# Optimization experiments

Hardware: AMD Instinct MI355X
Metric: run time of the kernel (lower is better)

The kernel has to match this reference:

```python
import jax, jax.numpy as jnp
import numpy as np


def setup_inputs() -> dict:
    key = jax.random.key(0)
    ks = jax.random.split(key, 6)
    N, D, E = 512, 16, 12
    X = jax.random.normal(ks[0], (N, D), jnp.float32)
    Y = jax.random.normal(ks[1], (N, E), jnp.float32)
    m = jax.random.normal(ks[2], (1, D), jnp.float32)
    A = jax.random.normal(ks[3], (D, D), jnp.float32)
    s = A @ A.T / D + 0.5 * jnp.eye(D, dtype=jnp.float32)  # SPD state covariance
    lengthscale = 0.5 + 1.5 * jax.random.uniform(ks[4], (E, D), jnp.float32)  # ARD lengthscales [E,D]
    outputscale = jnp.full((E,), 0.001, jnp.float32)  # Interval(0.001, 0.001001) constraint
    noise = 0.05 + 0.1 * jax.random.uniform(ks[5], (E,), jnp.float32)
    return {"X": X, "Y": Y, "m": m, "s": s,
            "lengthscale": lengthscale, "outputscale": outputscale, "noise": noise}


def _moment_match(X, Y, m, s, lengthscale, outputscale, noise):
    N, D = X.shape
    E = Y.shape[1]
    eyeD = jnp.eye(D, dtype=X.dtype)
    eyeN = jnp.eye(N, dtype=X.dtype)

    # --- standardization (torch std is unbiased, ddof=1) ---
    X_mean = jnp.mean(X, axis=0, keepdims=True)           # [1,D]
    X_std = jnp.std(X, axis=0, ddof=1, keepdims=True)     # [1,D]
    Yt = Y.T                                              # [E,N]
    Y_mean = jnp.mean(Yt, axis=-1, keepdims=True)         # [E,1]
    Y_std = jnp.std(Yt, axis=-1, ddof=1, keepdims=True)   # [E,1]
    Xs = (X - X_mean) / X_std                             # [N,D]
    Yn = (Yt - Y_mean) / Y_std                            # [E,N]

    inv_s = jnp.linalg.inv(s)
    mm = (m - X_mean) / X_std                             # [1,D]
    ss = s / (X_std.T * X_std)                            # [D,D]

    # --- calculate_factorizations ---
    diff = Xs[:, None, :] - Xs[None, :, :]                # [N,N,D]
    sq = jnp.sum((diff[None, :, :, :] / lengthscale[:, None, None, :]) ** 2, -1)  # [E,N,N]
    K = outputscale[:, None, None] * jnp.exp(-0.5 * sq)   # [E,N,N]
    A = K + noise[:, None, None] * eyeN                   # [E,N,N]
    iK = jnp.linalg.solve(A, jnp.broadcast_to(eyeN, (E, N, N)))  # [E,N,N]
    beta = jnp.linalg.solve(A, Yn[:, :, None])[:, :, 0]   # [E,N]

    # --- predict_given_factorizations ---
    inp = Xs - mm                                         # [N,D] centralized inputs
    iN = inp[None, :, :] / lengthscale[:, None, :]        # [E,N,D]
    ls2 = lengthscale ** 2                                # [E,D]
    # B = iL @ s @ iL + I
    B = ss[None, :, :] / (lengthscale[:, :, None] * lengthscale[:, None, :]) + eyeD  # [E,D,D]
    t = jnp.swapaxes(jnp.linalg.solve(B, jnp.swapaxes(iN, 1, 2)), 1, 2)  # [E,N,D]
    lb = jnp.exp(-0.5 * jnp.sum(iN * t, -1)) * beta       # [E,N]
    tiL = t / lengthscale[:, None, :]                     # [E,N,D]
    c = outputscale / jnp.sqrt(jnp.linalg.det(B))         # [E]
    M = (jnp.sum(lb, -1) * c)[:, None]                    # [E,1]
    V = jnp.einsum('end,en->ed', tiL, lb) * c[:, None]    # [E,D]

    # cross terms over output pairs (a,b)
    R0diag = 1.0 / ls2[None, :, :] + 1.0 / ls2[:, None, :]          # [E,E,D]
    R = ss[None, None, :, :] * R0diag[:, :, None, :] + eyeD          # s @ diag(r) + I, [E,E,D,D]
    X1 = inp[None, None, :, :] / ls2[:, None, None, :]               # [E,1,N,D]
    X2 = -inp[None, None, :, :] / ls2[None, :, None, :]              # [1,E,N,D]
    Q = jnp.linalg.solve(R, jnp.broadcast_to(ss, (E, E, D, D))) / 2  # [E,E,D,D]
    X1Q = X1 @ Q                                                     # [E,E,N,D]
    X2Q = X2 @ Q                                                     # [E,E,N,D]
    Xs_ = jnp.sum(X1Q * X1, -1)                                      # [E,E,N]
    X2s = jnp.sum(X2Q * X2, -1)                                      # [E,E,N]
    maha = -2.0 * (X1Q @ jnp.swapaxes(jnp.broadcast_to(X2, (E, E, N, D)), -1, -2)) \
        + Xs_[:, :, :, None] + X2s[:, :, None, :]                    # [E,E,N,N]
    kvec = jnp.log(outputscale)[:, None] - 0.5 * jnp.sum(iN ** 2, -1)  # [E,N]
    L = jnp.exp(kvec[:, None, :, None] + kvec[None, :, None, :] + maha)  # [E,E,N,N]
    S = jnp.einsum('an,abnm,bm->ab', beta, L, beta)                  # [E,E]
    diagL = L[jnp.arange(E), jnp.arange(E)]                          # [E,N,N]
    S = S - jnp.diag(jnp.sum(iK * diagL, axis=(1, 2)))
    S = S / jnp.sqrt(jnp.linalg.det(R))
    S = S + jnp.diag(outputscale)
    S = S - M @ M.T

    Mout = M.T                                                       # [1,E]
    Vout = V.T                                                       # [D,E]

    # --- de-standardize ---
    Mout = Mout * Y_std.T + Y_mean.T
    S = S * (Y_std * Y_std.T)
    var = jnp.concatenate([X_std, Y_std.T], axis=-1)                 # [1,D+E]
    mask_var = var.T * var                                           # [D+E,D+E]
    cov = (ss @ Vout) * mask_var[:D, D:]                             # [D,E]
    Vout = inv_s @ cov
    return Mout, S, Vout


def reference(X, Y, m, s, lengthscale, outputscale, noise):
    return _moment_match(X, Y, m, s, lengthscale, outputscale, noise)
```

## Files before the change

kernel.cpp:

```cpp
#include <hip/hip_runtime.h>
#include <math.h>

constexpr int N = 512;
constexpr int D = 16;
constexpr int E = 12;
constexpr int NPAIR = E*(E+1)/2;

constexpr size_t OFF_A     = 0;
constexpr size_t OFF_IK    = OFF_A    + (size_t)E*N*N;
constexpr size_t OFF_XS    = OFF_IK   + (size_t)E*N*N;
constexpr size_t OFF_INP   = OFF_XS   + (size_t)N*D;
constexpr size_t OFF_YN    = OFF_INP  + (size_t)N*D;
constexpr size_t OFF_BETA  = OFF_YN   + (size_t)E*N;
constexpr size_t OFF_KVEC  = OFF_BETA + (size_t)E*N;
constexpr size_t OFF_LB    = OFF_KVEC + (size_t)E*N;
constexpr size_t OFF_TIL   = OFF_LB   + (size_t)E*N;
constexpr size_t OFF_U     = OFF_TIL  + (size_t)E*N*D;
constexpr size_t OFF_V     = OFF_U    + (size_t)E*E*N;
constexpr size_t OFF_Q     = OFF_V    + (size_t)E*E*N;
constexpr size_t OFF_BINV  = OFF_Q    + (size_t)E*E*D*D;
constexpr size_t OFF_C     = OFF_BINV + (size_t)E*D*D;
constexpr size_t OFF_ISDR  = OFF_C    + E;
constexpr size_t OFF_SPART = OFF_ISDR + E*E;
constexpr size_t OFF_TPART = OFF_SPART+ (size_t)E*E*8;
constexpr size_t OFF_XMEAN = OFF_TPART+ (size_t)E*8;
constexpr size_t OFF_XSTD  = OFF_XMEAN+ D;
constexpr size_t OFF_YMEAN = OFF_XSTD + D;
constexpr size_t OFF_YSTD  = OFF_YMEAN+ E;
constexpr size_t OFF_SSM   = OFF_YSTD + E;
constexpr size_t OFF_P     = OFF_SSM  + D*D;
constexpr size_t OFF_T     = OFF_P    + (size_t)E*1792*64;

__device__ __forceinline__ int prow(int k) { return k*(480 - 32*k); }

__device__ __forceinline__ void pc2ab(int pc, int& a, int& b) {
    int aa = 0, t = pc;
    while (t >= E - aa) { t -= E - aa; ++aa; }
    a = aa; b = aa + t;
}

__device__ __forceinline__ void fact64(float a[16], float (*cb)[64], float* invd, int lane, int wv) {
    #pragma unroll
    for (int k = 0; k < 64; ++k) {
        const int kg = k >> 4, kj = k & 15;
        if (wv == kg) {
            float dkk = __shfl(a[kj], k);
            float dv = sqrtf(dkk);
            float iv = 1.0f / dv;
            float sc = a[kj] * iv;
            if (lane == k)      { a[kj] = dv; invd[k] = iv; }
            else if (lane > k)  a[kj] = sc;
            cb[k & 1][lane] = (lane > k) ? a[kj] : 0.0f;
        }
        __syncthreads();
        float lrk = cb[k & 1][lane];
        #pragma unroll
        for (int j = 0; j < 16; ++j)
            a[j] = fmaf(-lrk, cb[k & 1][wv*16 + j], a[j]);
    }
}

__device__ __forceinline__ void binv64(const float (*Lsh)[65], float (*Xsh)[65],
                                       const float* invd, float (*Tsh)[16][17], int tid) {
    if (tid < 64) {
        int g = tid >> 4, c = tid & 15;
        int b = g*16;
        for (int r = 0; r < c; ++r) Xsh[b+r][b+c] = 0.f;
        for (int r = c; r < 16; ++r) {
            float acc = (r == c) ? 1.0f : 0.0f;
            for (int k = c; k < r; ++k)
                acc = fmaf(-Lsh[b+r][b+k], Xsh[b+k][b+c], acc);
            Xsh[b+r][b+c] = acc * invd[b+r];
        }
    } else {
        const int bis[6] = {0,0,0,1,1,2};
        const int bjs[6] = {1,2,3,2,3,3};
        for (int idx = tid - 64; idx < 1536; idx += 192) {
            int blk = idx >> 8, off = idx & 255;
            Xsh[bis[blk]*16 + (off >> 4)][bjs[blk]*16 + (off & 15)] = 0.f;
        }
    }
    __syncthreads();
    for (int d = 1; d <= 3; ++d) {
        int np = 4 - d;
        for (int idx = tid; idx < np*256; idx += 256) {
            int p = idx >> 8, off = idx & 255;
            int r = off >> 4, c = off & 15;
            int i = p + d, j = p;
            float acc = 0.f;
            for (int k = j; k < i; ++k)
                #pragma unroll
                for (int m = 0; m < 16; ++m)
                    acc = fmaf(Lsh[i*16+r][k*16+m], Xsh[k*16+m][j*16+c], acc);
            Tsh[p][r][c] = acc;
        }
        __syncthreads();
        for (int idx = tid; idx < np*256; idx += 256) {
            int p = idx >> 8, off = idx & 255;
            int r = off >> 4, c = off & 15;
            int i = p + d, j = p;
            float acc = 0.f;
            #pragma unroll
            for (int m = 0; m < 16; ++m)
                acc = fmaf(Xsh[i*16+r][i*16+m], Tsh[p][m][c], acc);
            Xsh[i*16+r][j*16+c] = -acc;
        }
        __syncthreads();
    }
}

__device__ __forceinline__ void load_tile4(const float* __restrict__ g, size_t ldg,
                                           float (*S)[65], int tid) {
    #pragma unroll
    for (int j = 0; j < 4; ++j) {
        int idx = tid + j*256;
        int r = idx >> 4, c4 = idx & 15;
        float4 v = *(const float4*)&g[(size_t)r*ldg + c4*4];
        S[r][c4*4+0] = v.x; S[r][c4*4+1] = v.y; S[r][c4*4+2] = v.z; S[r][c4*4+3] = v.w;
    }
}

__device__ __forceinline__ void xs_body(float* __restrict__ ws, const float* __restrict__ ls,
                                        const float* __restrict__ os, int t, int tid) {
    int pc = t / N, n = t % N;
    int a, b;
    pc2ab(pc, a, b);
    int pairQ = a*E + b;
    __shared__ float Qs[16][17];
    __shared__ float i2a[16], i2b[16];
    Qs[tid >> 4][tid & 15] = ws[OFF_Q + (size_t)pairQ*D*D + tid];
    if (tid < 16) { float l = ls[a*D + tid]; i2a[tid] = 1.0f/(l*l); }
    else if (tid < 32) { int d = tid-16; float l = ls[b*D + d]; i2b[d] = 1.0f/(l*l); }
    __syncthreads();
    float x1[D], x2[D];
    float siNa = 0.f, siNb = 0.f;
    #pragma unroll
    for (int d = 0; d < D; ++d) {
        float ip = ws[OFF_INP + n*D + d];
        x1[d] = ip * i2a[d];
        x2[d] = ip * i2b[d];
        siNa = fmaf(ip*ip, i2a[d], siNa);
        siNb = fmaf(ip*ip, i2b[d], siNb);
    }
    float xs1 = 0.f, xs2 = 0.f;
    #pragma unroll
    for (int j = 0; j < D; ++j) {
        float t1 = 0.f, t2 = 0.f;
        #pragma unroll
        for (int i = 0; i < D; ++i) { t1 = fmaf(x1[i], Qs[i][j], t1); t2 = fmaf(x2[i], Qs[i][j], t2); }
        xs1 = fmaf(t1, x1[j], xs1);
        xs2 = fmaf(t2, x2[j], xs2);
    }
    float loa = logf(os[a]), lob = logf(os[b]);
    ws[OFF_U + (size_t)pc*N + n] = loa - 0.5f*siNa + xs1;
    ws[OFF_V + (size_t)pc*N + n] = lob - 0.5f*siNb + xs2;
}

__device__ __forceinline__ void point_body(float* __restrict__ ws, const float* __restrict__ ls,
                                           int t) {
    int e = t >> 9, n = t & 511;
    float iN[D], tt[D], l[D];
    #pragma unroll
    for (int d = 0; d < D; ++d) { l[d] = ls[e*D + d]; iN[d] = ws[OFF_INP + n*D + d] / l[d]; }
    #pragma unroll
    for (int d = 0; d < D; ++d) {
        float acc = 0.f;
        #pragma unroll
        for (int j = 0; j < D; ++j) acc += ws[OFF_BINV + ((size_t)e*D + d)*D + j] * iN[j];
        tt[d] = acc;
    }
    float siNt = 0.f;
    #pragma unroll
    for (int d = 0; d < D; ++d) siNt += iN[d]*tt[d];
    float lbv = __expf(-0.5f * siNt) * ws[OFF_BETA + e*N + n];
    ws[OFF_LB + e*N + n] = lbv;
    #pragma unroll
    for (int d = 0; d < D; ++d) ws[OFF_TIL + ((size_t)e*N + n)*D + d] = tt[d] / l[d];
}

__global__ __launch_bounds__(512) void k_prep(const float* __restrict__ X, const float* __restrict__ Y,
                                              const float* __restrict__ m, const float* __restrict__ s,
                                              float* __restrict__ ws) {
    int tid = threadIdx.x;
    int lane = tid & 63, wave = tid >> 6;
    __shared__ float meanX[D], stdX[D], meanY[E], stdY[E], mmsh[D];

    for (int col = wave; col < D + E; col += 8) {
        float s1 = 0.f, s2 = 0.f;
        if (col < D) {
            #pragma unroll
            for (int i = 0; i < 8; ++i) { float v = X[(i*64 + lane)*D + col]; s1 += v; s2 += v*v; }
        } else {
            int e = col - D;
            #pragma unroll
            for (int i = 0; i < 8; ++i) { float v = Y[(i*64 + lane)*E + e]; s1 += v; s2 += v*v; }
        }
        #pragma unroll
        for (int off = 32; off > 0; off >>= 1) { s1 += __shfl_xor(s1, off); s2 += __shfl_xor(s2, off); }
        if (lane == 0) {
            float mean = s1 * (1.0f/N);
            float var  = (s2 - (float)N*mean*mean) * (1.0f/(N-1));
            float sd   = sqrtf(var);
            if (col < D) { meanX[col] = mean; stdX[col] = sd; }
            else         { meanY[col-D] = mean; stdY[col-D] = sd; }
        }
    }
    __syncthreads();
    if (tid < D) {
        mmsh[tid] = (m[tid] - meanX[tid]) / stdX[tid];
        ws[OFF_XMEAN + tid] = meanX[tid];
        ws[OFF_XSTD  + tid] = stdX[tid];
    }
    if (tid < E) { ws[OFF_YMEAN + tid] = meanY[tid]; ws[OFF_YSTD + tid] = stdY[tid]; }
    __syncthreads();
    int n = tid;
    #pragma unroll
    for (int d = 0; d < D; ++d) {
        float xs = (X[n*D + d] - meanX[d]) / stdX[d];
        ws[OFF_XS  + n*D + d] = xs;
        ws[OFF_INP + n*D + d] = xs - mmsh[d];
    }
    #pragma unroll
    for (int e = 0; e < E; ++e)
        ws[OFF_YN + e*N + n] = (Y[n*E + e] - meanY[e]) / stdY[e];
    if (tid < D*D) {
        int i = tid / D, j = tid % D;
        ws[OFF_SSM + tid] = s[tid] / (stdX[i] * stdX[j]);
    }
}

__global__ __launch_bounds__(256) void k_buildA(float* __restrict__ ws, const float* __restrict__ ls,
                                                const float* __restrict__ os, const float* __restrict__ noise) {
    int bid = blockIdx.x;
    int tid = threadIdx.x;
    if (bid < E*64) {
        int e  = bid >> 6;
        int t  = bid & 63;
        int bn = t >> 3, bm = t & 7;
        __shared__ float xn[64][17], xm[64][17];
        __shared__ float il2[16];
        for (int idx = tid; idx < 1024; idx += 256) {
            int r = idx >> 4, d0 = idx & 15;
            xn[r][d0] = ws[OFF_XS + (size_t)(bn*64 + r)*D + d0];
            xm[r][d0] = ws[OFF_XS + (size_t)(bm*64 + r)*D + d0];
        }
        if (tid < 16) { float l = ls[e*D + tid]; il2[tid] = 1.0f/(l*l); }
        __syncthreads();
        int tx = tid & 15, ty = tid >> 4;
        float osv = os[e], nsv = noise[e];
        float acc[4][4] = {};
        #pragma unroll
        for (int d = 0; d < 16; ++d) {
            float il = il2[d];
            float an[4], am[4];
            #pragma unroll
            for (int q = 0; q < 4; ++q) { an[q] = xn[ty + q*16][d]; am[q] = xm[tx + q*16][d]; }
            #pragma unroll
            for (int q = 0; q < 4; ++q)
                #pragma unroll
                for (int w = 0; w < 4; ++w) { float df = an[q] - am[w]; acc[q][w] = fmaf(df*df, il, acc[q][w]); }
        }
        float* A = ws + OFF_A + (size_t)e*N*N;
        #pragma unroll
        for (int q = 0; q < 4; ++q)
            #pragma unroll
            for (int w = 0; w < 4; ++w) {
                int nr = bn*64 + ty + q*16, mc = bm*64 + tx + w*16;
                float v = osv * __expf(-0.5f * acc[q][w]);
                if (nr == mc) v += nsv;
                A[(size_t)nr*N + mc] = v;
            }
        return;
    }
    int bidx = bid - E*64;
    int i = tid >> 4, j = tid & 15;
    if (bidx < E) {
        int e = bidx;
        __shared__ float Bm[16][17], BInv[16][17];
        float li = ls[e*D + i], lj = ls[e*D + j];
        Bm[i][j] = ws[OFF_SSM + i*D + j] / (li*lj) + ((i==j) ? 1.f : 0.f);
        BInv[i][j] = (i==j) ? 1.f : 0.f;
        __syncthreads();
        float det = 1.f;
        for (int k = 0; k < D; ++k) {
            float p   = Bm[k][k];
            float fik = Bm[i][k];
            float bkj = Bm[k][j];
            float ikj = BInv[k][j];
            __syncthreads();
            det *= p;
            if (i == k) { Bm[k][j] = bkj/p; BInv[k][j] = ikj/p; }
            else        { float f = fik/p; Bm[i][j] -= f*bkj; BInv[i][j] -= f*ikj; }
            __syncthreads();
        }
        ws[OFF_BINV + ((size_t)e*D + i)*D + j] = BInv[i][j];
        if (tid == 0) ws[OFF_C + e] = os[e] / sqrtf(det);
    } else {
        int pair = bidx - E;
        int a = pair / E, b = pair % E;
        __shared__ float Rm[16][17], RInv[16][17], ssl[16][17];
        float la = ls[a*D + j], lb2 = ls[b*D + j];
        float rj = 1.f/(la*la) + 1.f/(lb2*lb2);
        float ssv = ws[OFF_SSM + i*D + j];
        ssl[i][j] = ssv;
        Rm[i][j] = ssv * rj + ((i==j) ? 1.f : 0.f);
        RInv[i][j] = (i==j) ? 1.f : 0.f;
        __syncthreads();
        float det = 1.f;
        for (int k = 0; k < D; ++k) {
            float p   = Rm[k][k];
            float fik = Rm[i][k];
            float rkj = Rm[k][j];
            float ikj = RInv[k][j];
            __syncthreads();
            det *= p;
            if (i == k) { Rm[k][j] = rkj/p; RInv[k][j] = ikj/p; }
            else        { float f = fik/p; Rm[i][j] -= f*rkj; RInv[i][j] -= f*ikj; }
            __syncthreads();
        }
        float q = 0.f;
        #pragma unroll
        for (int k2 = 0; k2 < D; ++k2) q += RInv[i][k2] * ssl[k2][j];
        ws[OFF_Q + ((size_t)pair*D + i)*D + j] = 0.5f * q;
        if (tid == 0) ws[OFF_ISDR + pair] = 1.f / sqrtf(det);
    }
}

__global__ __launch_bounds__(256) void k_diag64(float* __restrict__ ws, int k0) {
    int e = blockIdx.x;
    int tid = threadIdx.x;
    int lane = tid & 63, wv = tid >> 6;
    const float* A = ws + OFF_A + (size_t)e*N*N;
    float* W = ws + OFF_IK + (size_t)e*N*N;
    __shared__ float Lsh[64][65], Xsh[64][65];
    __shared__ float cb[2][64];
    __shared__ float invd[64];
    __shared__ float Tsh[3][16][17];
    float a[16];
    #pragma unroll
    for (int j = 0; j < 16; ++j)
        a[j] = A[(size_t)(k0 + wv*16 + j)*N + k0 + lane];
    __syncthreads();
    fact64(a, cb, invd, lane, wv);
    #pragma unroll
    for (int j = 0; j < 16; ++j) Lsh[lane][wv*16 + j] = a[j];
    __syncthreads();
    binv64(Lsh, Xsh, invd, Tsh, tid);
    for (int idx = tid; idx < 4096; idx += 256) {
        int r = idx >> 6, c = idx & 63;
        W[(size_t)(k0 + r)*N + k0 + c] = Xsh[r][c];
    }
}

__global__ __launch_bounds__(256) void k_panelmul(float* __restrict__ ws, int k0) {
    int kk = k0 >> 6;
    int nb = (N - k0 - 64) >> 6;
    int e  = blockIdx.x / nb;
    int bi = blockIdx.x % nb;
    float* A = ws + OFF_A + (size_t)e*N*N;
    const float* W = ws + OFF_IK + (size_t)e*N*N;
    int r0 = k0 + 64 + bi*64;
    __shared__ float Ps[64][65], Wsh[64][65];
    int tid = threadIdx.x;
    load_tile4(A + (size_t)r0*N + k0, N, Ps, tid);
    load_tile4(W + (size_t)k0*N + k0, N, Wsh, tid);
    __syncthreads();
    int tx = tid & 15, ty = tid >> 4;
    float acc[4][4] = {};
    #pragma unroll 8
    for (int j = 0; j < 64; ++j) {
        float pr[4], wr[4];
        #pragma unroll
        for (int q = 0; q < 4; ++q) { pr[q] = Ps[ty*4+q][j]; wr[q] = Wsh[tx*4+q][j]; }
        #pragma unroll
        for (int q = 0; q < 4; ++q)
            #pragma unroll
            for (int w = 0; w < 4; ++w) acc[q][w] = fmaf(pr[q], wr[w], acc[q][w]);
    }
    float* Pp = ws + OFF_P + ((size_t)e*1792 + prow(kk) + (size_t)bi*64)*64;
    #pragma unroll
    for (int q = 0; q < 4; ++q)
        #pragma unroll
        for (int w = 0; w < 4; ++w) {
            A[(size_t)(r0 + ty*4 + q)*N + k0 + tx*4 + w] = acc[q][w];
            Pp[(size_t)(ty*4 + q)*64 + tx*4 + w] = acc[q][w];
        }
}

__global__ __launch_bounds__(256) void k_traild(float* __restrict__ ws, int k0) {
    int t0 = k0 + 64;
    int nb = (N - t0) >> 6;
    int ntiles = (nb*(nb+1)) >> 1;
    int e = blockIdx.x / ntiles;
    int t = blockIdx.x % ntiles;
    int bj = 0; while (t >= nb - bj) { t -= nb - bj; ++bj; }
    int bi = bj + t;
    bool same = (bi == bj);
    bool isdiag0 = (bi == 0) && (bj == 0);
    float* A = ws + OFF_A + (size_t)e*N*N;
    __shared__ float Sr[64][65], Sc[64][65];
    __shared__ float cb[2][64];
    __shared__ float invd[64];
    __shared__ float Tsh[3][16][17];
    int tid = threadIdx.x;
    int tx = tid & 15, ty = tid >> 4;
    load_tile4(A + (size_t)(t0 + bi*64)*N + k0, N, Sr, tid);
    if (!same) load_tile4(A + (size_t)(t0 + bj*64)*N + k0, N, Sc, tid);
    __syncthreads();
    float acc[4][4] = {};
    if (same) {
        #pragma unroll 8
        for (int p = 0; p < 64; ++p) {
            float ar[4], ac[4];
            #pragma unroll
            for (int q = 0; q < 4; ++q) { ar[q] = Sr[ty*4+q][p]; ac[q] = Sr[tx*4+q][p]; }
            #pragma unroll
            for (int q = 0; q < 4; ++q)
                #pragma unroll
                for (int w = 0; w < 4; ++w) acc[q][w] = fmaf(ar[q], ac[w], acc[q][w]);
        }
    } else {
        #pragma unroll 8
        for (int p = 0; p < 64; ++p) {
            float ar[4], ac[4];
            #pragma unroll
            for (int q = 0; q < 4; ++q) { ar[q] = Sr[ty*4+q][p]; ac[q] = Sc[tx*4+q][p]; }
            #pragma unroll
            for (int q = 0; q < 4; ++q)
                #pragma unroll
                for (int w = 0; w < 4; ++w) acc[q][w] = fmaf(ar[q], ac[w], acc[q][w]);
        }
    }
    float* Out = A + (size_t)(t0 + bi*64)*N + (t0 + bj*64);
    if (!isdiag0) {
        #pragma unroll
        for (int q = 0; q < 4; ++q)
            #pragma unroll
            for (int w = 0; w < 4; ++w)
                Out[(size_t)(ty*4+q)*N + tx*4+w] -= acc[q][w];
        return;
    }
    __syncthreads();
    #pragma unroll
    for (int q = 0; q < 4; ++q)
        #pragma unroll
        for (int w = 0; w < 4; ++w)
            Sc[ty*4+q][tx*4+w] = Out[(size_t)(ty*4+q)*N + tx*4+w] - acc[q][w];
    __syncthreads();
    int lane = tid & 63, wv = tid >> 6;
    float a[16];
    #pragma unroll
    for (int j = 0; j < 16; ++j) a[j] = Sc[lane][wv*16 + j];
    __syncthreads();
    fact64(a, cb, invd, lane, wv);
    #pragma unroll
    for (int j = 0; j < 16; ++j) Sc[lane][wv*16 + j] = a[j];
    __syncthreads();
    binv64(Sc, Sr, invd, Tsh, tid);
    float* W = ws + OFF_IK + (size_t)e*N*N;
    for (int idx = tid; idx < 4096; idx += 256) {
        int r = idx >> 6, c = idx & 63;
        W[(size_t)(t0 + r)*N + t0 + c] = Sr[r][c];
    }
}

__global__ __launch_bounds__(256) void k_dc1(float* __restrict__ ws) {
    int e = blockIdx.x >> 2, p = blockIdx.x & 3;
    float* W = ws + OFF_IK + (size_t)e*N*N;
    const float* Lt = ws + OFF_P + ((size_t)e*1792 + prow(2*p))*64;
    __shared__ float Sa[64][65], Sb[64][65], T[64][65];
    int tid = threadIdx.x;
    int tx = tid & 15, ty = tid >> 4;
    load_tile4(Lt, 64, Sa, tid);
    load_tile4(W + (size_t)(2*p*64)*N + 2*p*64, N, Sb, tid);
    __syncthreads();
    float acc[4][4] = {};
    #pragma unroll 8
    for (int pp = 0; pp < 64; ++pp) {
        float ar[4], bc[4];
        #pragma unroll
        for (int q = 0; q < 4; ++q) { ar[q] = Sa[ty*4+q][pp]; bc[q] = Sb[pp][tx*4+q]; }
        #pragma unroll
        for (int q = 0; q < 4; ++q)
            #pragma unroll
            for (int w = 0; w < 4; ++w) acc[q][w] = fmaf(ar[q], bc[w], acc[q][w]);
    }
    #pragma unroll
    for (int q = 0; q < 4; ++q)
        #pragma unroll
        for (int w = 0; w < 4; ++w) T[ty*4+q][tx*4+w] = acc[q][w];
    __syncthreads();
    load_tile4(W + (size_t)((2*p+1)*64)*N + (2*p+1)*64, N, Sa, tid);
    __syncthreads();
    float o[4][4] = {};
    #pragma unroll 8
    for (int pp = 0; pp < 64; ++pp) {
        float ar[4], bc[4];
        #pragma unroll
        for (int q = 0; q < 4; ++q) { ar[q] = Sa[ty*4+q][pp]; bc[q] = T[pp][tx*4+q]; }
        #pragma unroll
        for (int q = 0; q < 4; ++q)
            #pragma unroll
            for (int w = 0; w < 4; ++w) o[q][w] = fmaf(ar[q], bc[w], o[q][w]);
    }
    #pragma unroll
    for (int q = 0; q < 4; ++q)
        #pragma unroll
        for (int w = 0; w < 4; ++w)
            W[(size_t)((2*p+1)*64 + ty*4 + q)*N + 2*p*64 + tx*4 + w] = -o[q][w];
}

__global__ __launch_bounds__(256) void k_dcT(float* __restrict__ ws, int H) {
    int per_e = 4*H;
    int e = blockIdx.x / per_e;
    int rem = blockIdx.x % per_e;
    int p  = rem / (H*H);
    int tt = rem % (H*H);
    int ti = tt / H, tj = tt % H;
    int C0 = 2*p*H;
    int I  = C0 + H + ti;
    const float* W = ws + OFF_IK + (size_t)e*N*N;
    float* Tt = ws + OFF_T + (size_t)e*65536 + (size_t)(p*H*H + ti*H + tj)*4096;
    __shared__ float Sa[64][65], Sb[64][65];
    int tid = threadIdx.x;
    int tx = tid & 15, ty = tid >> 4;
    float acc[4][4] = {};
    for (int k = tj; k < H; ++k) {
        int K = C0 + k;
        const float* Lt = ws + OFF_P + ((size_t)e*1792 + prow(K) + (size_t)(I - K - 1)*64)*64;
        __syncthreads();
        load_tile4(Lt, 64, Sa, tid);
        load_tile4(W + (size_t)(K*64)*N + (C0 + tj)*64, N, Sb, tid);
        __syncthreads();
        #pragma unroll 8
        for (int pp = 0; pp < 64; ++pp) {
            float ar[4], bc[4];
            #pragma unroll
            for (int q = 0; q < 4; ++q) { ar[q] = Sa[ty*4+q][pp]; bc[q] = Sb[pp][tx*4+q]; }
            #pragma unroll
            for (int q = 0; q < 4; ++q)
                #pragma unroll
                for (int w = 0; w < 4; ++w) acc[q][w] = fmaf(ar[q], bc[w], acc[q][w]);
        }
    }
    #pragma unroll
    for (int q = 0; q < 4; ++q)
        #pragma unroll
        for (int w = 0; w < 4; ++w)
            Tt[(size_t)(ty*4+q)*64 + tx*4 + w] = acc[q][w];
}

__global__ __launch_bounds__(256) void k_dcW(float* __restrict__ ws, int H) {
    int per_e = 4*H;
    int e = blockIdx.x / per_e;
    int rem = blockIdx.x % per_e;
    int p  = rem / (H*H);
    int tt = rem % (H*H);
    int ti = tt / H, tj = tt % H;
    int C0 = 2*p*H, R0 = C0 + H;
    float* W = ws + OFF_IK + (size_t)e*N*N;
    const float* Tbase = ws + OFF_T + (size_t)e*65536 + (size_t)(p*H*H)*4096;
    __shared__ float Sa[64][65], Sb[64][65];
    int tid = threadIdx.x;
    int tx = tid & 15, ty = tid >> 4;
    float acc[4][4] = {};
    for (int tk = 0; tk <= ti; ++tk) {
        const float* Tt = Tbase + (size_t)(tk*H + tj)*4096;
        __syncthreads();
        load_tile4(W + (size_t)((R0 + ti)*64)*N + (R0 + tk)*64, N, Sa, tid);
        load_tile4(Tt, 64, Sb, tid);
        __syncthreads();
        #pragma unroll 8
        for (int pp = 0; pp < 64; ++pp) {
            float ar[4], bc[4];
            #pragma unroll
            for (int q = 0; q < 4; ++q) { ar[q] = Sa[ty*4+q][pp]; bc[q] = Sb[pp][tx*4+q]; }
            #pragma unroll
            for (int q = 0; q < 4; ++q)
                #pragma unroll
                for (int w = 0; w < 4; ++w) acc[q][w] = fmaf(ar[q], bc[w], acc[q][w]);
        }
    }
    #pragma unroll
    for (int q = 0; q < 4; ++q)
        #pragma unroll
        for (int w = 0; w < 4; ++w)
            W[(size_t)((R0 + ti)*64 + ty*4 + q)*N + (C0 + tj)*64 + tx*4 + w] = -acc[q][w];
}

__global__ __launch_bounds__(256) void k_syrk(float* __restrict__ ws, const float* __restrict__ ls,
                                              const float* __restrict__ os) {
    int tid = threadIdx.x;
    if (blockIdx.x >= E*36) {
        int t = (blockIdx.x - E*36)*256 + tid;
        xs_body(ws, ls, os, t, tid);
        return;
    }
    int e = blockIdx.x / 36;
    int t = blockIdx.x % 36;
    int bj = 0; while (t >= 8 - bj) { t -= 8 - bj; ++bj; }
    int bi = bj + t;
    bool same = (bi == bj);
    const float* W = ws + OFF_IK + (size_t)e*N*N;
    float*      IK = ws + OFF_A  + (size_t)e*N*N;
    __shared__ float Sa[64][65], Sb[64][65];
    int tx = tid & 15, ty = tid >> 4;

    float4 pa[4], pb[4];
    #pragma unroll
    for (int j = 0; j < 4; ++j) {
        int idx = tid + j*256;
        int r = idx >> 4, c4 = idx & 15;
        pa[j] = *(const float4*)&W[(size_t)(bi*64 + r)*N + bi*64 + c4*4];
        if (!same) pb[j] = *(const float4*)&W[(size_t)(bi*64 + r)*N + bj*64 + c4*4];
    }

    float acc[4][4] = {};
    for (int p = bi; p < 8; ++p) {
        __syncthreads();
        #pragma unroll
        for (int j = 0; j < 4; ++j) {
            int idx = tid + j*256;
            int r = idx >> 4, c4 = idx & 15;
            Sa[r][c4*4+0] = pa[j].x; Sa[r][c4*4+1] = pa[j].y; Sa[r][c4*4+2] = pa[j].z; Sa[r][c4*4+3] = pa[j].w;
            if (!same) { Sb[r][c4*4+0] = pb[j].x; Sb[r][c4*4+1] = pb[j].y; Sb[r][c4*4+2] = pb[j].z; Sb[r][c4*4+3] = pb[j].w; }
        }
        if (p < 7) {
            #pragma unroll
            for (int j = 0; j < 4; ++j) {
                int idx = tid + j*256;
                int r = idx >> 4, c4 = idx & 15;
                pa[j] = *(const float4*)&W[(size_t)((p+1)*64 + r)*N + bi*64 + c4*4];
                if (!same) pb[j] = *(const float4*)&W[(size_t)((p+1)*64 + r)*N + bj*64 + c4*4];
            }
        }
        __syncthreads();
        if (same) {
            #pragma unroll 8
            for (int pr2 = 0; pr2 < 64; ++pr2) {
                float ar[4], ac[4];
                #pragma unroll
                for (int q = 0; q < 4; ++q) { ar[q] = Sa[pr2][ty*4+q]; ac[q] = Sa[pr2][tx*4+q]; }
                #pragma unroll
                for (int q = 0; q < 4; ++q)
                    #pragma unroll
                    for (int w = 0; w < 4; ++w) acc[q][w] = fmaf(ar[q], ac[w], acc[q][w]);
            }
        } else {
            #pragma unroll 8
            for (int pr2 = 0; pr2 < 64; ++pr2) {
                float ar[4], ac[4];
                #pragma unroll
                for (int q = 0; q < 4; ++q) { ar[q] = Sa[pr2][ty*4+q]; ac[q] = Sb[pr2][tx*4+q]; }
                #pragma unroll
                for (int q = 0; q < 4; ++q)
                    #pragma unroll
                    for (int w = 0; w < 4; ++w) acc[q][w] = fmaf(ar[q], ac[w], acc[q][w]);
            }
        }
    }
    #pragma unroll
    for (int q = 0; q < 4; ++q)
        #pragma unroll
        for (int w = 0; w < 4; ++w) {
            int r = bi*64 + ty*4 + q, c = bj*64 + tx*4 + w;
            IK[(size_t)r*N + c] = acc[q][w];
            IK[(size_t)c*N + r] = acc[q][w];
        }
}

__global__ __launch_bounds__(256) void k_beta(float* __restrict__ ws) {
    int e = blockIdx.x >> 2, qtr = blockIdx.x & 3;
    int tid = threadIdx.x;
    int half = tid >> 7;
    int nl = tid & 127;
    int n = qtr*128 + nl;
    __shared__ float yn[N];
    __shared__ float part[2][128];
    for (int i = tid; i < N; i += 256) yn[i] = ws[OFF_YN + (size_t)e*N + i];
    __syncthreads();
    const float* IK = ws + OFF_A + (size_t)e*N*N;
    int m0 = half*256;
    float a0 = 0.f, a1 = 0.f, a2 = 0.f, a3 = 0.f;
    for (int mm = m0; mm < m0 + 256; mm += 4) {
        a0 = fmaf(IK[(size_t)mm*N + n],     yn[mm],   a0);
        a1 = fmaf(IK[(size_t)(mm+1)*N + n], yn[mm+1], a1);
        a2 = fmaf(IK[(size_t)(mm+2)*N + n], yn[mm+2], a2);
        a3 = fmaf(IK[(size_t)(mm+3)*N + n], yn[mm+3], a3);
    }
    part[half][nl] = (a0 + a1) + (a2 + a3);
    __syncthreads();
    if (tid < 128)
        ws[OFF_BETA + e*N + qtr*128 + tid] = part[0][tid] + part[1][tid];
}

__global__ __launch_bounds__(256) void k_S(float* __restrict__ ws, const float* __restrict__ ls,
                                           const float* __restrict__ os) {
    int tid = threadIdx.x;
    if (blockIdx.x >= NPAIR*8) {
        int t = (blockIdx.x - NPAIR*8)*256 + tid;
        point_body(ws, ls, t);
        return;
    }
    int bid = blockIdx.x;
    int pc = bid >> 3, ntile = bid & 7;
    int a, b;
    pc2ab(pc, a, b);
    int pairQ = a*E + b;
    int tx = tid & 15, ty = tid >> 4;
    __shared__ float Qs[16][17];
    __shared__ float i2a[16], i2b[16];
    __shared__ float __align__(16) bufAT[16][68];
    __shared__ float __align__(16) x1qT[16][68];
    __shared__ float __align__(16) bufBT[16][68];
    __shared__ float u_s[64], v_s[64], ba_s[64], bb_s[64];
    __shared__ float red[256];
    int n0 = ntile*64;
    Qs[tid >> 4][tid & 15] = ws[OFF_Q + (size_t)pairQ*D*D + tid];
    if (tid < 16) { float l = ls[a*D + tid]; i2a[tid] = 1.0f/(l*l); }
    else if (tid < 32) { int d = tid-16; float l = ls[b*D + d]; i2b[d] = 1.0f/(l*l); }
    __syncthreads();
    for (int idx = tid; idx < 1024; idx += 256) {
        int r = idx >> 4, d = idx & 15;
        bufAT[d][r] = ws[OFF_INP + (size_t)(n0 + r)*D + d] * i2a[d];
    }
    __syncthreads();
    for (int idx = tid; idx < 1024; idx += 256) {
        int r = idx >> 4, j = idx & 15;
        float s = 0.f;
        #pragma unroll
        for (int i = 0; i < 16; ++i) s = fmaf(bufAT[i][r], Qs[i][j], s);
        x1qT[j][r] = s;
    }
    if (tid < 64) {
        u_s[tid]  = ws[OFF_U + (size_t)pc*N + n0 + tid];
        ba_s[tid] = ws[OFF_BETA + a*N + n0 + tid];
    }
    __syncthreads();
    float4 av4[16];
    #pragma unroll
    for (int d = 0; d < 16; ++d) av4[d] = *(const float4*)&x1qT[d][ty*4];
    float uq[4], baq[4];
    #pragma unroll
    for (int q = 0; q < 4; ++q) { uq[q] = u_s[ty*4+q]; baq[q] = ba_s[ty*4+q]; }

    float pf[4];
    #pragma unroll
    for (int j = 0; j < 4; ++j) {
        int idx = tid + j*256;
        pf[j] = ws[OFF_INP + (size_t)((idx >> 4))*D + (idx & 15)];
    }
    float vpf = 0.f, bpf = 0.f;
    if (tid < 64) {
        vpf = ws[OFF_V + (size_t)pc*N + tid];
        bpf = ws[OFF_BETA + b*N + tid];
    }

    float sacc = 0.f, tacc = 0.f;
    for (int mt = 0; mt < 8; ++mt) {
        __syncthreads();
        #pragma unroll
        for (int j = 0; j < 4; ++j) {
            int idx = tid + j*256;
            bufBT[idx & 15][idx >> 4] = pf[j] * i2b[idx & 15];
        }
        if (tid < 64) { v_s[tid] = vpf; bb_s[tid] = bpf; }
        if (mt < 7) {
            #pragma unroll
            for (int j = 0; j < 4; ++j) {
                int idx = tid + j*256;
                pf[j] = ws[OFF_INP + (size_t)((mt+1)*64 + (idx >> 4))*D + (idx & 15)];
            }
            if (tid < 64) {
                vpf = ws[OFF_V + (size_t)pc*N + (mt+1)*64 + tid];
                bpf = ws[OFF_BETA + b*N + (mt+1)*64 + tid];
            }
        }
        __syncthreads();
        float dacc[4][4] = {};
        #pragma unroll
        for (int d = 0; d < 16; ++d) {
            float4 bv = *(const float4*)&bufBT[d][tx*4];
            float4 av = av4[d];
            dacc[0][0] = fmaf(av.x, bv.x, dacc[0][0]); dacc[0][1] = fmaf(av.x, bv.y, dacc[0][1]);
            dacc[0][2] = fmaf(av.x, bv.z, dacc[0][2]); dacc[0][3] = fmaf(av.x, bv.w, dacc[0][3]);
            dacc[1][0] = fmaf(av.y, bv.x, dacc[1][0]); dacc[1][1] = fmaf(av.y, bv.y, dacc[1][1]);
            dacc[1][2] = fmaf(av.y, bv.z, dacc[1][2]); dacc[1][3] = fmaf(av.y, bv.w, dacc[1][3]);
            dacc[2][0] = fmaf(av.z, bv.x, dacc[2][0]); dacc[2][1] = fmaf(av.z, bv.y, dacc[2][1]);
            dacc[2][2] = fmaf(av.z, bv.z, dacc[2][2]); dacc[2][3] = fmaf(av.z, bv.w, dacc[2][3]);
            dacc[3][0] = fmaf(av.w, bv.x, dacc[3][0]); dacc[3][1] = fmaf(av.w, bv.y, dacc[3][1]);
            dacc[3][2] = fmaf(av.w, bv.z, dacc[3][2]); dacc[3][3] = fmaf(av.w, bv.w, dacc[3][3]);
        }
        #pragma unroll
        for (int q = 0; q < 4; ++q) {
            float ikq[4];
            if (a == b)
                *(float4*)ikq = *(const float4*)&ws[OFF_A + ((size_t)a*N + n0 + ty*4 + q)*N + mt*64 + tx*4];
            #pragma unroll
            for (int w = 0; w < 4; ++w) {
                float Lv = __expf(2.f*dacc[q][w] + uq[q] + v_s[tx*4+w]);
                sacc = fmaf(baq[q] * bb_s[tx*4+w], Lv, sacc);
                if (a == b)
                    tacc = fmaf(ikq[w], Lv, tacc);
            }
        }
    }
    red[tid] = sacc; __syncthreads();
    for (int o = 128; o > 0; o >>= 1) { if (tid < o) red[tid] += red[tid+o]; __syncthreads(); }
    if (tid == 0) ws[OFF_SPART + bid] = red[0];
    if (a == b) {
        __syncthreads();
        red[tid] = tacc; __syncthreads();
        for (int o = 128; o > 0; o >>= 1) { if (tid < o) red[tid] += red[tid+o]; __syncthreads(); }
        if (tid == 0) ws[OFF_TPART + a*8 + ntile] = red[0];
    }
}

__global__ __launch_bounds__(256) void k_final(float* __restrict__ ws, const float* __restrict__ s,
                                               const float* __restrict__ os, float* __restrict__ out) {
    int tid = threadIdx.x;
    __shared__ float Msh[E], Vsh[E][D], cov[D][E+1];
    __shared__ float Sm[16][17], Si[16][17];
    __shared__ float vred[16][17];

    {
        int wv = tid >> 6, lane = tid & 63;
        for (int e = wv; e < E; e += 4) {
            float sum = 0.f;
            #pragma unroll
            for (int i = 0; i < 8; ++i) sum += ws[OFF_LB + e*N + i*64 + lane];
            #pragma unroll
            for (int off = 32; off > 0; off >>= 1) sum += __shfl_xor(sum, off);
            if (lane == 0) Msh[e] = ws[OFF_C + e] * sum;
        }
    }
    for (int e = 0; e < E; ++e) {
        int d = tid & 15, sl = tid >> 4;
        float acc = 0.f;
        for (int i = 0; i < 32; ++i) {
            int n = sl*32 + i;
            acc = fmaf(ws[OFF_TIL + ((size_t)e*N + n)*D + d], ws[OFF_LB + e*N + n], acc);
        }
        vred[sl][d] = acc;
        __syncthreads();
        if (tid < 16) {
            float sum = 0.f;
            #pragma unroll
            for (int s2 = 0; s2 < 16; ++s2) sum += vred[s2][tid];
            Vsh[e][tid] = ws[OFF_C + e] * sum;
        }
        __syncthreads();
    }

    if (tid < E*E) {
        int a = tid / E, bb = tid % E;
        int amin = (a < bb) ? a : bb;
        int amax = (a < bb) ? bb : a;
        int pc = amin*E - (amin*(amin-1))/2 + (amax - amin);
        float acc = 0.f;
        for (int q = 0; q < 8; ++q) acc += ws[OFF_SPART + (size_t)pc*8 + q];
        if (a == bb) {
            float tr = 0.f;
            for (int q = 0; q < 8; ++q) tr += ws[OFF_TPART + a*8 + q];
            acc -= tr;
        }
        acc *= ws[OFF_ISDR + tid];
        if (a == bb) acc += os[a];
        float v = acc - Msh[a]*Msh[bb];
        v *= ws[OFF_YSTD + a] * ws[OFF_YSTD + bb];
        out[E + tid] = v;
    }
    if (tid < E) out[tid] = Msh[tid]*ws[OFF_YSTD + tid] + ws[OFF_YMEAN + tid];

    if (tid < D*E) {
        int d = tid / E, e = tid % E;
        float acc = 0.f;
        for (int k = 0; k < D; ++k) acc += ws[OFF_SSM + d*D + k] * Vsh[e][k];
        cov[d][e] = acc * ws[OFF_XSTD + d] * ws[OFF_YSTD + e];
    }
    int i = tid >> 4, j = tid & 15;
    Sm[i][j] = s[i*D + j];
    Si[i][j] = (i==j) ? 1.f : 0.f;
    __syncthreads();
    for (int k = 0; k < D; ++k) {
        float p   = Sm[k][k];
        float fik = Sm[i][k];
        float skj = Sm[k][j];
        float ikj = Si[k][j];
        __syncthreads();
        if (i == k) { Sm[k][j] = skj/p; Si[k][j] = ikj/p; }
        else        { float f = fik/p; Sm[i][j] -= f*skj; Si[i][j] -= f*ikj; }
        __syncthreads();
    }
    if (tid < D*E) {
        int d = tid / E, e = tid % E;
        float acc = 0.f;
        for (int k = 0; k < D; ++k) acc += Si[d][k] * cov[k][e];
        out[E + E*E + d*E + e] = acc;
    }
}

extern "C" void kernel_launch(void* const* d_in, const int* in_sizes, int n_in,
                              void* d_out, int out_size, void* d_ws, size_t ws_size,
                              hipStream_t stream) {
    const float* X     = (const float*)d_in[0];
    const float* Y     = (const float*)d_in[1];
    const float* m     = (const float*)d_in[2];
    const float* s     = (const float*)d_in[3];
    const float* ls    = (const float*)d_in[4];
    const float* os    = (const float*)d_in[5];
    const float* noise = (const float*)d_in[6];
    float* ws  = (float*)d_ws;
    float* out = (float*)d_out;

    k_prep   <<<1,              512, 0, stream>>>(X, Y, m, s, ws);
    k_buildA <<<E*64 + E + E*E, 256, 0, stream>>>(ws, ls, os, noise);
    k_diag64 <<<E,              256, 0, stream>>>(ws, 0);
    for (int kk = 0; kk < 7; ++kk) {
        int k0 = kk*64;
        int nb = 7 - kk;
        k_panelmul<<<E*nb,          256, 0, stream>>>(ws, k0);
        k_traild  <<<E*nb*(nb+1)/2, 256, 0, stream>>>(ws, k0);
    }
    k_dc1 <<<E*4,  256, 0, stream>>>(ws);
    k_dcT <<<E*8,  256, 0, stream>>>(ws, 2);
    k_dcW <<<E*8,  256, 0, stream>>>(ws, 2);
    k_dcT <<<E*16, 256, 0, stream>>>(ws, 4);
    k_dcW <<<E*16, 256, 0, stream>>>(ws, 4);
    k_syrk <<<E*36 + NPAIR*N/256,   256, 0, stream>>>(ws, ls, os);
    k_beta <<<E*4,                  256, 0, stream>>>(ws);
    k_S    <<<NPAIR*8 + E*N/256,    256, 0, stream>>>(ws, ls, os);
    k_final<<<1,                    256, 0, stream>>>(ws, s, os, out);
}
```

Before: 517.3 us.

## Fuse panel multiply into trailing update kernel of blocked Cholesky inverse

Removes the separate k_panelmul launch at each of the 7 block steps. Each trailing-update block now loads the inverted diagonal tile and recomputes the panel products for its own row and column tiles in shared memory before the rank-64 update. Blocks with bj==0 also write the panel product to the P buffer. This saves 7 dependent kernel launches and one global round trip of the panel, at the cost of redundant panel GEMMs and more shared memory per block. The panel result is no longer written back into A, so correctness depends on nothing later reading those entries.

```diff
diff --git a/kernel.cpp b/kernel.cpp
--- a/kernel.cpp
+++ b/kernel.cpp
@@ -352,42 +352,8 @@
     }
 }
 
-__global__ __launch_bounds__(256) void k_panelmul(float* __restrict__ ws, int k0) {
+__global__ __launch_bounds__(256) void k_traild(float* __restrict__ ws, int k0) {
     int kk = k0 >> 6;
-    int nb = (N - k0 - 64) >> 6;
-    int e  = blockIdx.x / nb;
-    int bi = blockIdx.x % nb;
-    float* A = ws + OFF_A + (size_t)e*N*N;
-    const float* W = ws + OFF_IK + (size_t)e*N*N;
-    int r0 = k0 + 64 + bi*64;
-    __shared__ float Ps[64][65], Wsh[64][65];
-    int tid = threadIdx.x;
-    load_tile4(A + (size_t)r0*N + k0, N, Ps, tid);
-    load_tile4(W + (size_t)k0*N + k0, N, Wsh, tid);
-    __syncthreads();
-    int tx = tid & 15, ty = tid >> 4;
-    float acc[4][4] = {};
-    #pragma unroll 8
-    for (int j = 0; j < 64; ++j) {
-        float pr[4], wr[4];
-        #pragma unroll
-        for (int q = 0; q < 4; ++q) { pr[q] = Ps[ty*4+q][j]; wr[q] = Wsh[tx*4+q][j]; }
-        #pragma unroll
-        for (int q = 0; q < 4; ++q)
-            #pragma unroll
-            for (int w = 0; w < 4; ++w) acc[q][w] = fmaf(pr[q], wr[w], acc[q][w]);
-    }
-    float* Pp = ws + OFF_P + ((size_t)e*1792 + prow(kk) + (size_t)bi*64)*64;
-    #pragma unroll
-    for (int q = 0; q < 4; ++q)
-        #pragma unroll
-        for (int w = 0; w < 4; ++w) {
-            A[(size_t)(r0 + ty*4 + q)*N + k0 + tx*4 + w] = acc[q][w];
-            Pp[(size_t)(ty*4 + q)*64 + tx*4 + w] = acc[q][w];
-        }
-}
-
-__global__ __launch_bounds__(256) void k_traild(float* __restrict__ ws, int k0) {
     int t0 = k0 + 64;
     int nb = (N - t0) >> 6;
     int ntiles = (nb*(nb+1)) >> 1;
@@ -398,15 +364,66 @@
     bool same = (bi == bj);
     bool isdiag0 = (bi == 0) && (bj == 0);
     float* A = ws + OFF_A + (size_t)e*N*N;
-    __shared__ float Sr[64][65], Sc[64][65];
+    const float* Wd = ws + OFF_IK + (size_t)e*N*N;
+    __shared__ float Wsh[64][65], Sr[64][65], Sc[64][65];
     __shared__ float cb[2][64];
     __shared__ float invd[64];
     __shared__ float Tsh[3][16][17];
     int tid = threadIdx.x;
     int tx = tid & 15, ty = tid >> 4;
+
+    load_tile4(Wd + (size_t)k0*N + k0, N, Wsh, tid);
     load_tile4(A + (size_t)(t0 + bi*64)*N + k0, N, Sr, tid);
     if (!same) load_tile4(A + (size_t)(t0 + bj*64)*N + k0, N, Sc, tid);
     __syncthreads();
+    float pr[4][4] = {}, pc[4][4] = {};
+    if (same) {
+        #pragma unroll 8
+        for (int j = 0; j < 64; ++j) {
+            float w4[4], a4[4];
+            #pragma unroll
+            for (int q = 0; q < 4; ++q) { w4[q] = Wsh[tx*4+q][j]; a4[q] = Sr[ty*4+q][j]; }
+            #pragma unroll
+            for (int q = 0; q < 4; ++q)
+                #pragma unroll
+                for (int w = 0; w < 4; ++w) pr[q][w] = fmaf(a4[q], w4[w], pr[q][w]);
+        }
+    } else {
+        #pragma unroll 4
+        for (int j = 0; j < 64; ++j) {
+            float w4[4], a4[4], c4[4];
+            #pragma unroll
+            for (int q = 0; q < 4; ++q) { w4[q] = Wsh[tx*4+q][j]; a4[q] = Sr[ty*4+q][j]; c4[q] = Sc[ty*4+q][j]; }
+            #pragma unroll
+            for (int q = 0; q < 4; ++q)
+                #pragma unroll
+                for (int w = 0; w < 4; ++w) {
+                    pr[q][w] = fmaf(a4[q], w4[w], pr[q][w]);
+                    pc[q][w] = fmaf(c4[q], w4[w], pc[q][w]);
+                }
+        }
+    }
+    __syncthreads();
+    #pragma unroll
+    for (int q = 0; q < 4; ++q)
+        #pragma unroll
+        for (int w = 0; w < 4; ++w) Sr[ty*4+q][tx*4+w] = pr[q][w];
+    if (!same) {
+        #pragma unroll
+        for (int q = 0; q < 4; ++q)
+            #pragma unroll
+            for (int w = 0; w < 4; ++w) Sc[ty*4+q][tx*4+w] = pc[q][w];
+    }
+    __syncthreads();
+    if (bj == 0) {
+        float* Pp = ws + OFF_P + ((size_t)e*1792 + prow(kk) + (size_t)bi*64)*64;
+        #pragma unroll
+        for (int j = 0; j < 4; ++j) {
+            int idx = tid + j*256;
+            int r = idx >> 6, c = idx & 63;
+            Pp[(size_t)r*64 + c] = Sr[r][c];
+        }
+    }
     float acc[4][4] = {};
     if (same) {
         #pragma unroll 8
@@ -917,10 +934,8 @@
     k_buildA <<<E*64 + E + E*E, 256, 0, stream>>>(ws, ls, os, noise);
     k_diag64 <<<E,              256, 0, stream>>>(ws, 0);
     for (int kk = 0; kk < 7; ++kk) {
-        int k0 = kk*64;
         int nb = 7 - kk;
-        k_panelmul<<<E*nb,          256, 0, stream>>>(ws, k0);
-        k_traild  <<<E*nb*(nb+1)/2, 256, 0, stream>>>(ws, k0);
+        k_traild<<<E*nb*(nb+1)/2, 256, 0, stream>>>(ws, kk*64);
     }
     k_dc1 <<<E*4,  256, 0, stream>>>(ws);
     k_dcT <<<E*8,  256, 0, stream>>>(ws, 2);
```

Measured after the change: 492.3 us. 1.05x faster.
